# Kernel tuning notes

Hardware: AMD Instinct MI355X
Metric: run time of the kernel (lower is better)

The kernel has to match this reference:

```python
import jax, jax.numpy as jnp
import numpy as np

B, T, C, K = 16, 4096, 64, 1024  # K = codebook rows including pad row 0


def setup_inputs() -> dict:
    key = jax.random.key(0)
    k1, k2, k3 = jax.random.split(key, 3)
    z = jax.random.normal(k1, (B, T, C), dtype=jnp.float32)
    codebook_weight = jax.random.normal(k2, (K, C), dtype=jnp.float32)
    # contiguous valid prefixes of random length (torch loop breaks at first 0)
    lengths = jax.random.randint(k3, (B,), T // 2, T + 1)
    mask = (jnp.arange(T)[None, :] < lengths[:, None]).astype(jnp.float32)[:, :, None]
    return {"z": z, "codebook_weight": codebook_weight, "mask": mask}


def _forward(z, codebook_weight, mask):
    # F.normalize(z, p=2, dim=-1) with eps clamp
    z = z / jnp.clip(jnp.linalg.norm(z, axis=-1, keepdims=True), 1e-12)
    e = jax.lax.stop_gradient(codebook_weight)[1:]  # (K-1, C), detached like torch
    zf = z.reshape(-1, C)                            # (B*T, C)
    # squared euclidean distances: ||z||^2 + ||e||^2 - 2 z e^T
    d = (zf * zf).sum(1, keepdims=True) + (e * e).sum(1)[None, :] - 2.0 * (zf @ e.T)
    idx = jnp.argmin(d, axis=1).reshape(B, T)        # (B, T) codes in [0, K-2]
    # scatter(one-hot) @ e  ==  gather rows of e
    z_q = e[idx] * mask                              # (B, T, C)

    valid_count = mask.sum()
    commitment_loss = (jnp.square(z - jax.lax.stop_gradient(z_q)) * mask).sum() / valid_count

    # straight-through estimator
    z_q = z + z_q - jax.lax.stop_gradient(z)

    m1 = mask[:, 1:, :]
    smoothness_loss = (jnp.square(z_q[:, :-1, :] - z_q[:, 1:, :]) * m1).sum() / m1.sum()

    # --- parallel RLE (replaces the host-side python loop) ---
    # torch loop breaks at first mask==0 -> only contiguous valid prefix matters
    mvalid = jnp.cumprod(mask[..., 0], axis=1) > 0   # (B, T) bool
    change = idx[:, 1:] != idx[:, :-1]
    # position 0 always starts a segment; new segment where code changes inside valid prefix
    is_start = jnp.concatenate(
        [jnp.ones((B, 1), dtype=bool), change & mvalid[:, 1:]], axis=1)  # (B, T)
    # stable argsort puts start positions first, in increasing time order
    order = jnp.argsort(jnp.where(is_start, 0, 1), axis=1)               # (B, T)
    n = is_start.sum(axis=1)                                             # segments per batch
    sel_mask = jnp.arange(T)[None, :] < n[:, None]                        # (B, T)
    sel_pos = jnp.where(sel_mask, order, 0)                               # padded to T
    n_mask = sel_mask.astype(jnp.float32)[..., None]                      # (B, T, 1)
    n_z_q = jnp.take_along_axis(z_q, sel_pos[:, :, None], axis=1) * n_mask
    selected_encodings = jnp.where(
        sel_mask, jnp.take_along_axis(idx, sel_pos, axis=1) + 1, 0)       # (B, T) int
    return smoothness_loss, commitment_loss, z_q, n_z_q, n_mask, selected_encodings


def reference(z, codebook_weight, mask):
    return _forward(z, codebook_weight, mask)
```

## Files before the change

### kernel.cpp

```cpp
#include <hip/hip_runtime.h>
#include <math.h>

typedef __attribute__((ext_vector_type(8))) short short8;
typedef __attribute__((ext_vector_type(4))) float f32x4;

#define B_  16
#define T_  4096
#define C_  64
#define KE_ 1023
#define BT_ (B_ * T_)
#define WINDOW 1e-3f


__device__ __forceinline__ unsigned short f2bf(float x) {
    unsigned int u = __float_as_uint(x);
    unsigned int r = (u + 0x7FFFu + ((u >> 16) & 1u)) >> 16;
    return (unsigned short)r;
}
__device__ __forceinline__ float bf2f(unsigned short h) {
    return __uint_as_float(((unsigned int)h) << 16);
}

__global__ __launch_bounds__(256) void k_prep(const float* __restrict__ cb,
                                              float* __restrict__ ee,
                                              unsigned short* __restrict__ Eh,
                                              unsigned short* __restrict__ El,
                                              int* __restrict__ flagcnt) {
    const int k = blockIdx.x * 256 + threadIdx.x;
    if (k == 0) *flagcnt = 0;
    unsigned int* EhU = (unsigned int*)Eh;
    unsigned int* ElU = (unsigned int*)El;
    if (k < KE_) {
        const float* r = cb + (size_t)(k + 1) * C_;
        float s = 0.f;
        #pragma unroll
        for (int c = 0; c < C_; c += 2) {
            const float x0 = r[c], x1 = r[c + 1];
            s = fmaf(x0, x0, s);
            s = fmaf(x1, x1, s);
            const unsigned short h0 = f2bf(x0), h1 = f2bf(x1);
            const unsigned short l0 = f2bf(x0 - bf2f(h0));
            const unsigned short l1 = f2bf(x1 - bf2f(h1));
            EhU[k * 32 + c / 2] = (unsigned int)h0 | ((unsigned int)h1 << 16);
            ElU[k * 32 + c / 2] = (unsigned int)l0 | ((unsigned int)l1 << 16);
        }
        ee[k] = s;
    } else {
        #pragma unroll
        for (int c = 0; c < 32; ++c) { EhU[k * 32 + c] = 0u; ElU[k * 32 + c] = 0u; }
        ee[k] = INFINITY;
    }
}

__global__ __launch_bounds__(256, 4) void k_assign(
    const float* __restrict__ z, const unsigned short* __restrict__ Eh,
    const unsigned short* __restrict__ El, const float* __restrict__ ee,
    int* __restrict__ kbest, int* __restrict__ flaglist,
    int* __restrict__ flagcnt) {

    __shared__ __align__(16) unsigned short s_eh[128 * 72];
    __shared__ __align__(16) unsigned short s_el[128 * 72];
    __shared__ float s_ee[128];

    const int tid  = threadIdx.x;
    const int wave = tid >> 6;
    const int lane = tid & 63;
    const int col  = lane & 15;
    const int quad = lane >> 4;
    const int Q0   = blockIdx.x * 128 + wave * 32;

    short8 ah[2][2], al[2][2];
    #pragma unroll
    for (int g = 0; g < 2; ++g) {
        const float4* zp = (const float4*)(z + (size_t)(Q0 + g * 16 + col) * C_);
        const float4 f0 = zp[quad * 2];
        const float4 f1 = zp[quad * 2 + 1];
        const float4 f2 = zp[8 + quad * 2];
        const float4 f3 = zp[8 + quad * 2 + 1];
        float xs[16] = {f0.x, f0.y, f0.z, f0.w, f1.x, f1.y, f1.z, f1.w,
                        f2.x, f2.y, f2.z, f2.w, f3.x, f3.y, f3.z, f3.w};
        float ss = 0.f;
        #pragma unroll
        for (int i = 0; i < 16; ++i) ss = fmaf(xs[i], xs[i], ss);
        ss += __shfl_xor(ss, 16);
        ss += __shfl_xor(ss, 32);
        const float inv = 1.f / fmaxf(sqrtf(ss), 1e-12f);
        short8 h0, h1, l0, l1;
        #pragma unroll
        for (int i = 0; i < 8; ++i) {
            const float x = xs[i] * inv;
            const unsigned short hx = f2bf(x);
            h0[i] = (short)hx;
            l0[i] = (short)f2bf(x - bf2f(hx));
            const float y = xs[8 + i] * inv;
            const unsigned short hy = f2bf(y);
            h1[i] = (short)hy;
            l1[i] = (short)f2bf(y - bf2f(hy));
        }
        ah[g][0] = h0; ah[g][1] = h1;
        al[g][0] = l0; al[g][1] = l1;
    }

    float bestv[2][4], secv[2][4];
    int   bkk[2][4];
    #pragma unroll
    for (int g = 0; g < 2; ++g)
        #pragma unroll
        for (int r = 0; r < 4; ++r) {
            bestv[g][r] = INFINITY; secv[g][r] = INFINITY; bkk[g][r] = 0;
        }

    for (int t = 0; t < 8; ++t) {
        __syncthreads();
        #pragma unroll
        for (int j = 0; j < 4; ++j) {
            const int p   = j * 256 + tid;
            const int row = p >> 3;
            const int pc  = p & 7;
            *(uint4*)(&s_eh[row * 72 + pc * 8]) =
                *(const uint4*)(&Eh[(size_t)(t * 128 + row) * 64 + pc * 8]);
            *(uint4*)(&s_el[row * 72 + pc * 8]) =
                *(const uint4*)(&El[(size_t)(t * 128 + row) * 64 + pc * 8]);
        }
        if (tid < 128) s_ee[tid] = ee[t * 128 + tid];
        __syncthreads();

        #pragma unroll 2
        for (int s = 0; s < 8; ++s) {
            const int rbase = (s * 16 + col) * 72 + quad * 8;
            const short8 bh0 = *(const short8*)(&s_eh[rbase]);
            const short8 bh1 = *(const short8*)(&s_eh[rbase + 32]);
            const short8 bl0 = *(const short8*)(&s_el[rbase]);
            const short8 bl1 = *(const short8*)(&s_el[rbase + 32]);
            const float  eev = s_ee[s * 16 + col];

            f32x4 p0 = {0.f, 0.f, 0.f, 0.f}, q0 = {0.f, 0.f, 0.f, 0.f};
            f32x4 p1 = {0.f, 0.f, 0.f, 0.f}, q1 = {0.f, 0.f, 0.f, 0.f};
            p0 = __builtin_amdgcn_mfma_f32_16x16x32_bf16(ah[0][0], bh0, p0, 0, 0, 0);
            p1 = __builtin_amdgcn_mfma_f32_16x16x32_bf16(ah[1][0], bh0, p1, 0, 0, 0);
            q0 = __builtin_amdgcn_mfma_f32_16x16x32_bf16(ah[0][1], bh1, q0, 0, 0, 0);
            q1 = __builtin_amdgcn_mfma_f32_16x16x32_bf16(ah[1][1], bh1, q1, 0, 0, 0);
            p0 = __builtin_amdgcn_mfma_f32_16x16x32_bf16(ah[0][0], bl0, p0, 0, 0, 0);
            p1 = __builtin_amdgcn_mfma_f32_16x16x32_bf16(ah[1][0], bl0, p1, 0, 0, 0);
            q0 = __builtin_amdgcn_mfma_f32_16x16x32_bf16(ah[0][1], bl1, q0, 0, 0, 0);
            q1 = __builtin_amdgcn_mfma_f32_16x16x32_bf16(ah[1][1], bl1, q1, 0, 0, 0);
            p0 = __builtin_amdgcn_mfma_f32_16x16x32_bf16(al[0][0], bh0, p0, 0, 0, 0);
            p1 = __builtin_amdgcn_mfma_f32_16x16x32_bf16(al[1][0], bh0, p1, 0, 0, 0);
            q0 = __builtin_amdgcn_mfma_f32_16x16x32_bf16(al[0][1], bh1, q0, 0, 0, 0);
            q1 = __builtin_amdgcn_mfma_f32_16x16x32_bf16(al[1][1], bh1, q1, 0, 0, 0);

            const int kc = t * 128 + s * 16 + col;
            #pragma unroll
            for (int r = 0; r < 4; ++r) {
                {
                    const float v = fmaf(-2.f, p0[r] + q0[r], eev);
                    const bool lt = v < bestv[0][r];
                    secv[0][r]  = lt ? bestv[0][r] : fminf(secv[0][r], v);
                    bkk[0][r]   = lt ? kc : bkk[0][r];
                    bestv[0][r] = lt ? v : bestv[0][r];
                }
                {
                    const float v = fmaf(-2.f, p1[r] + q1[r], eev);
                    const bool lt = v < bestv[1][r];
                    secv[1][r]  = lt ? bestv[1][r] : fminf(secv[1][r], v);
                    bkk[1][r]   = lt ? kc : bkk[1][r];
                    bestv[1][r] = lt ? v : bestv[1][r];
                }
            }
        }
    }

    #pragma unroll
    for (int g = 0; g < 2; ++g) {
        #pragma unroll
        for (int r = 0; r < 4; ++r) {
            float b  = bestv[g][r], sc = secv[g][r];
            int   k  = bkk[g][r];
            #pragma unroll
            for (int off = 1; off < 16; off <<= 1) {
                const float ob = __shfl_xor(b, off);
                const int   ok = __shfl_xor(k, off);
                const float os = __shfl_xor(sc, off);
                const bool take = (ob < b) || (ob == b && ok < k);
                const float lose = take ? b : ob;
                sc = fminf(fminf(sc, os), lose);
                b  = take ? ob : b;
                k  = take ? ok : k;
            }
            if (col == 0) {
                const int q = Q0 + g * 16 + quad * 4 + r;
                kbest[q] = k;
                if (!(sc - b > WINDOW)) {
                    const int pos = atomicAdd(flagcnt, 1);
                    flaglist[pos] = q;
                }
            }
        }
    }
}

__global__ __launch_bounds__(256) void k_fix(const float* __restrict__ z,
                                             const float* __restrict__ cb,
                                             const float* __restrict__ ee,
                                             const int* __restrict__ flagcnt,
                                             const int* __restrict__ flaglist,
                                             int* __restrict__ kbest) {
    __shared__ float s_z[64];
    __shared__ float s_bv[4];
    __shared__ int   s_bk[4];
    const int tid  = threadIdx.x;
    const int lane = tid & 63;
    const int wave = tid >> 6;
    const int n = *flagcnt;

    for (int i = blockIdx.x; i < n; i += 1024) {
        const int q = flaglist[i];
        __syncthreads();
        if (tid < 16) ((float4*)s_z)[tid] = ((const float4*)(z + (size_t)q * C_))[tid];
        __syncthreads();

        float4 zn[16];
        float ss = 0.f;
        #pragma unroll
        for (int c4 = 0; c4 < 16; ++c4) {
            const float4 v = ((const float4*)s_z)[c4];
            zn[c4] = v;
            ss = fmaf(v.x, v.x, ss); ss = fmaf(v.y, v.y, ss);
            ss = fmaf(v.z, v.z, ss); ss = fmaf(v.w, v.w, ss);
        }
        const float nrm = fmaxf(sqrtf(ss), 1e-12f);
        #pragma unroll
        for (int c4 = 0; c4 < 16; ++c4) {
            zn[c4].x /= nrm; zn[c4].y /= nrm; zn[c4].z /= nrm; zn[c4].w /= nrm;
        }

        const int k0 = tid * 4;
        const float4* e0 = (const float4*)(cb + (size_t)(k0 + 1) * C_);
        const float4* e1 = (const float4*)(cb + (size_t)(k0 + 2) * C_);
        const float4* e2 = (const float4*)(cb + (size_t)(k0 + 3) * C_);
        const float4* e3 = (const float4*)(cb + (size_t)((k0 + 4 <= KE_) ? (k0 + 4) : KE_) * C_);
        float d0 = 0.f, d1 = 0.f, d2 = 0.f, d3 = 0.f;
        #pragma unroll
        for (int c4 = 0; c4 < 16; ++c4) {
            const float4 x = zn[c4];
            const float4 a = e0[c4], b = e1[c4], c = e2[c4], d = e3[c4];
            d0 = fmaf(x.x, a.x, d0); d0 = fmaf(x.y, a.y, d0);
            d0 = fmaf(x.z, a.z, d0); d0 = fmaf(x.w, a.w, d0);
            d1 = fmaf(x.x, b.x, d1); d1 = fmaf(x.y, b.y, d1);
            d1 = fmaf(x.z, b.z, d1); d1 = fmaf(x.w, b.w, d1);
            d2 = fmaf(x.x, c.x, d2); d2 = fmaf(x.y, c.y, d2);
            d2 = fmaf(x.z, c.z, d2); d2 = fmaf(x.w, c.w, d2);
            d3 = fmaf(x.x, d.x, d3); d3 = fmaf(x.y, d.y, d3);
            d3 = fmaf(x.z, d.z, d3); d3 = fmaf(x.w, d.w, d3);
        }
        float bv = INFINITY;
        int   bk = 0;
        float v;
        v = fmaf(-2.f, d0, ee[k0 + 0]); if (v < bv) { bv = v; bk = k0 + 0; }
        v = fmaf(-2.f, d1, ee[k0 + 1]); if (v < bv) { bv = v; bk = k0 + 1; }
        v = fmaf(-2.f, d2, ee[k0 + 2]); if (v < bv) { bv = v; bk = k0 + 2; }
        v = fmaf(-2.f, d3, ee[k0 + 3]); if (v < bv) { bv = v; bk = k0 + 3; }

        #pragma unroll
        for (int off = 32; off > 0; off >>= 1) {
            const float ov = __shfl_down(bv, off);
            const int   ok = __shfl_down(bk, off);
            if (ov < bv || (ov == bv && ok < bk)) { bv = ov; bk = ok; }
        }
        if (lane == 0) { s_bv[wave] = bv; s_bk[wave] = bk; }
        __syncthreads();
        if (tid == 0) {
            float fb = s_bv[0]; int fk = s_bk[0];
            #pragma unroll
            for (int w = 1; w < 4; ++w) {
                if (s_bv[w] < fb || (s_bv[w] == fb && s_bk[w] < fk)) {
                    fb = s_bv[w]; fk = s_bk[w];
                }
            }
            kbest[q] = fk;
        }
    }
}

__global__ __launch_bounds__(256) void k_epi(
    const float* __restrict__ z, const float* __restrict__ cb,
    const float* __restrict__ mask, const int* __restrict__ kbest,
    float* __restrict__ zqo,
    float* __restrict__ commit_part, float* __restrict__ valid_part,
    float* __restrict__ smooth_part) {

    __shared__ float s_red[12];
    const int tid  = threadIdx.x;
    const int lane = tid & 63;
    const int wave = tid >> 6;
    const int q    = blockIdx.x * 256 + tid;

    const int bi = kbest[q];
    const float m     = mask[q];
    const float mnext = (lane != 63) ? mask[q + 1] : 0.f;

    const float4* zp = (const float4*)(z + (size_t)q * C_);
    const float4* er = (const float4*)(cb + (size_t)(bi + 1) * C_);
    float4* zo = (float4*)(zqo + (size_t)q * C_);

    float4 zr[16];
    float ss = 0.f;
    #pragma unroll
    for (int i = 0; i < 16; ++i) {
        float4 v = zp[i];
        zr[i] = v;
        ss = fmaf(v.x, v.x, ss); ss = fmaf(v.y, v.y, ss);
        ss = fmaf(v.z, v.z, ss); ss = fmaf(v.w, v.w, ss);
    }
    const float nrm = fmaxf(sqrtf(ss), 1e-12f);

    float commit = 0.f, sm = 0.f;
    #pragma unroll
    for (int c4 = 0; c4 < 16; ++c4) {
        const float z0 = zr[c4].x / nrm, z1 = zr[c4].y / nrm;
        const float z2 = zr[c4].z / nrm, z3 = zr[c4].w / nrm;
        const float4 e4 = er[c4];
        const float q0 = e4.x * m, q1 = e4.y * m, q2 = e4.z * m, q3 = e4.w * m;
        float4 o;
        o.x = (z0 + q0) - z0;
        o.y = (z1 + q1) - z1;
        o.z = (z2 + q2) - z2;
        o.w = (z3 + q3) - z3;
        zo[c4] = o;
        const float d0 = z0 - q0, d1 = z1 - q1, d2 = z2 - q2, d3 = z3 - q3;
        commit = fmaf(d0, d0, commit); commit = fmaf(d1, d1, commit);
        commit = fmaf(d2, d2, commit); commit = fmaf(d3, d3, commit);
        const float n0 = __shfl_down(o.x, 1);
        const float n1 = __shfl_down(o.y, 1);
        const float n2 = __shfl_down(o.z, 1);
        const float n3 = __shfl_down(o.w, 1);
        const float x0 = o.x - n0, x1 = o.y - n1;
        const float x2 = o.z - n2, x3 = o.w - n3;
        sm = fmaf(x0, x0, sm); sm = fmaf(x1, x1, sm);
        sm = fmaf(x2, x2, sm); sm = fmaf(x3, x3, sm);
    }
    commit *= m;
    sm     *= mnext;
    float vc = m;
    #pragma unroll
    for (int off = 32; off > 0; off >>= 1) {
        commit += __shfl_down(commit, off);
        vc     += __shfl_down(vc, off);
        sm     += __shfl_down(sm, off);
    }
    if (lane == 0) { s_red[wave] = commit; s_red[4 + wave] = vc; s_red[8 + wave] = sm; }
    __syncthreads();
    if (tid == 0) {
        commit_part[blockIdx.x] = s_red[0] + s_red[1] + s_red[2] + s_red[3];
        valid_part[blockIdx.x]  = s_red[4] + s_red[5] + s_red[6] + s_red[7];
        smooth_part[blockIdx.x] = s_red[8] + s_red[9] + s_red[10] + s_red[11];
    }
}

__global__ __launch_bounds__(256) void k_scan(const int* __restrict__ kbest,
                                              const float* __restrict__ mask,
                                              const float* __restrict__ zqo,
                                              int* __restrict__ selpos,
                                              int* __restrict__ nst,
                                              float* __restrict__ smooth_part) {
    __shared__ int cnt[256];
    __shared__ float sred[4];
    const int b = blockIdx.x;
    const int tid = threadIdx.x;
    const int base = b * T_;
    const int t0 = tid * 16;

    int flags = 0, c = 0;
    int prev = (tid == 0) ? -1 : kbest[base + t0 - 1];
    #pragma unroll
    for (int i = 0; i < 16; ++i) {
        const int t = t0 + i;
        const int cur = kbest[base + t];
        const int is = (t == 0) ? 1
                     : ((cur != prev && mask[base + t] > 0.f) ? 1 : 0);
        flags |= is << i;
        c += is;
        prev = cur;
    }
    cnt[tid] = c;
    __syncthreads();
    for (int off = 1; off < 256; off <<= 1) {
        int add = (tid >= off) ? cnt[tid - off] : 0;
        __syncthreads();
        cnt[tid] += add;
        __syncthreads();
    }
    int pos = cnt[tid] - c;
    #pragma unroll
    for (int i = 0; i < 16; ++i) {
        if ((flags >> i) & 1) selpos[base + pos++] = t0 + i;
    }
    if (tid == 255) nst[b] = cnt[255];

    float v = 0.f;
    for (int e = tid; e < 63 * 64; e += 256) {
        const int j = e >> 6, cc = e & 63;
        const int t = j * 64 + 63;
        const int qq = base + t;
        const float d = zqo[(size_t)qq * C_ + cc] - zqo[(size_t)(qq + 1) * C_ + cc];
        v = fmaf(d * mask[qq + 1], d, v);
    }
    #pragma unroll
    for (int off = 32; off > 0; off >>= 1) v += __shfl_down(v, off);
    if ((tid & 63) == 0) sred[tid >> 6] = v;
    __syncthreads();
    if (tid == 0) smooth_part[256 + b] = sred[0] + sred[1] + sred[2] + sred[3];
}

__global__ __launch_bounds__(256) void k_gsel(const float* __restrict__ zqo,
                                              const int* __restrict__ kbest,
                                              const int* __restrict__ selpos,
                                              const int* __restrict__ nst,
                                              const float* __restrict__ commit_part,
                                              const float* __restrict__ valid_part,
                                              const float* __restrict__ smooth_part,
                                              float* __restrict__ nzq,
                                              float* __restrict__ nmask,
                                              float* __restrict__ sel,
                                              float* __restrict__ out) {
    const int gid = blockIdx.x * 256 + threadIdx.x;
    const int b   = gid >> 16;
    const int rem = gid & 65535;
    const int j   = rem >> 4;
    const int c4  = rem & 15;
    const int n   = nst[b];
    float4 v = make_float4(0.f, 0.f, 0.f, 0.f);
    int p = 0;
    if (j < n) {
        p = selpos[b * T_ + j];
        v = ((const float4*)zqo)[((size_t)b * T_ + p) * 16 + c4];
    }
    ((float4*)nzq)[gid] = v;
    if (c4 == 0) {
        float nm = 0.f, s = 0.f;
        if (j < n) { nm = 1.f; s = (float)(kbest[b * T_ + p] + 1); }
        nmask[b * T_ + j] = nm;
        sel[b * T_ + j]   = s;
    }

    if (blockIdx.x == 0) {
        __shared__ double rc[256];
        __shared__ double rv[256];
        __shared__ double rs[256];
        const int tid = threadIdx.x;
        double sc = (double)commit_part[tid];
        double sv = (double)valid_part[tid];
        double ssm = (double)smooth_part[tid];
        if (tid < 16) ssm += (double)smooth_part[256 + tid];
        rc[tid] = sc; rv[tid] = sv; rs[tid] = ssm;
        __syncthreads();
        for (int off = 128; off > 0; off >>= 1) {
            if (tid < off) {
                rc[tid] += rc[tid + off];
                rv[tid] += rv[tid + off];
                rs[tid] += rs[tid + off];
            }
            __syncthreads();
        }
        if (tid == 0) {
            double valid = rv[0];
            out[0] = (float)(rs[0] / (valid - (double)B_));
            out[1] = (float)(rc[0] / valid);
        }
    }
}

extern "C" void kernel_launch(void* const* d_in, const int* in_sizes, int n_in,
                              void* d_out, int out_size, void* d_ws, size_t ws_size,
                              hipStream_t stream) {
    const float* z    = (const float*)d_in[0];
    const float* cb   = (const float*)d_in[1];
    const float* mask = (const float*)d_in[2];
    float* out = (float*)d_out;
    char* ws = (char*)d_ws;

    int*            flagcnt     = (int*)(ws + 0);
    float*          ee          = (float*)(ws + 64);
    unsigned short* Eh          = (unsigned short*)(ws + 4224);
    unsigned short* El          = (unsigned short*)(ws + 135296);
    int*            kbest       = (int*)(ws + 266368);
    int*            selpos      = (int*)(ws + 528512);
    int*            nst         = (int*)(ws + 790656);
    float*          commit_part = (float*)(ws + 791680);
    float*          valid_part  = (float*)(ws + 792704);
    float*          smooth_part = (float*)(ws + 793728);
    int*            flaglist    = (int*)(ws + 794816);

    float* zqo   = out + 2;
    float* nzq   = zqo + (size_t)BT_ * C_;
    float* nmask = nzq + (size_t)BT_ * C_;
    float* sel   = nmask + BT_;

    k_prep  <<<4,    256, 0, stream>>>(cb, ee, Eh, El, flagcnt);
    k_assign<<<512,  256, 0, stream>>>(z, Eh, El, ee, kbest, flaglist, flagcnt);
    k_fix   <<<1024, 256, 0, stream>>>(z, cb, ee, flagcnt, flaglist, kbest);
    k_epi   <<<256,  256, 0, stream>>>(z, cb, mask, kbest, zqo,
                                       commit_part, valid_part, smooth_part);
    k_scan  <<<B_,   256, 0, stream>>>(kbest, mask, zqo, selpos, nst, smooth_part);
    k_gsel  <<<4096, 256, 0, stream>>>(zqo, kbest, selpos, nst,
                                       commit_part, valid_part, smooth_part,
                                       nzq, nmask, sel, out);
}
```

Before: 155.7 us.

## Double-buffer codebook tiles via direct global-to-LDS loads and pack argmin keys

Codebook tiles are now prefetched into a second LDS buffer with global_load_lds while the current tile is consumed. The old padded rows are replaced by an XOR swizzle, and one barrier per tile is removed. The codebook is pre-negated and the MFMA accumulator starts at 0.5+0.5*||e||^2, so distances come out of the MFMA directly. Best and second-best tracking become unsigned min/max on keys that pack the positive float bits with the code index in the low 10 bits. This truncates distance precision, which is absorbed by a wider ambiguity window sent to the fixup kernel. It may flag more rows for the fix pass, and the doubled LDS lowers the occupancy hint to 2.

```diff
diff --git a/kernel.cpp b/kernel.cpp
--- a/kernel.cpp
+++ b/kernel.cpp
@@ -9,7 +9,7 @@
 #define C_  64
 #define KE_ 1023
 #define BT_ (B_ * T_)
-#define WINDOW 1e-3f
+#define WINHALF 0.01f
 
 
 __device__ __forceinline__ unsigned short f2bf(float x) {
@@ -21,8 +21,15 @@
     return __uint_as_float(((unsigned int)h) << 16);
 }
 
+typedef __attribute__((address_space(1))) const unsigned int g_u32;
+typedef __attribute__((address_space(3))) unsigned int l_u32;
+__device__ __forceinline__ void gload16(const void* g, void* l) {
+    __builtin_amdgcn_global_load_lds((g_u32*)g, (l_u32*)l, 16, 0, 0);
+}
+
 __global__ __launch_bounds__(256) void k_prep(const float* __restrict__ cb,
                                               float* __restrict__ ee,
+                                              float* __restrict__ ee2,
                                               unsigned short* __restrict__ Eh,
                                               unsigned short* __restrict__ El,
                                               int* __restrict__ flagcnt) {
@@ -38,29 +45,32 @@
             const float x0 = r[c], x1 = r[c + 1];
             s = fmaf(x0, x0, s);
             s = fmaf(x1, x1, s);
-            const unsigned short h0 = f2bf(x0), h1 = f2bf(x1);
-            const unsigned short l0 = f2bf(x0 - bf2f(h0));
-            const unsigned short l1 = f2bf(x1 - bf2f(h1));
+            const float n0 = -x0, n1 = -x1;
+            const unsigned short h0 = f2bf(n0), h1 = f2bf(n1);
+            const unsigned short l0 = f2bf(n0 - bf2f(h0));
+            const unsigned short l1 = f2bf(n1 - bf2f(h1));
             EhU[k * 32 + c / 2] = (unsigned int)h0 | ((unsigned int)h1 << 16);
             ElU[k * 32 + c / 2] = (unsigned int)l0 | ((unsigned int)l1 << 16);
         }
-        ee[k] = s;
+        ee[k]  = s;
+        ee2[k] = 0.5f + 0.5f * s;
     } else {
         #pragma unroll
         for (int c = 0; c < 32; ++c) { EhU[k * 32 + c] = 0u; ElU[k * 32 + c] = 0u; }
-        ee[k] = INFINITY;
-    }
-}
-
-__global__ __launch_bounds__(256, 4) void k_assign(
+        ee[k]  = INFINITY;
+        ee2[k] = INFINITY;
+    }
+}
+
+__global__ __launch_bounds__(256, 2) void k_assign(
     const float* __restrict__ z, const unsigned short* __restrict__ Eh,
-    const unsigned short* __restrict__ El, const float* __restrict__ ee,
+    const unsigned short* __restrict__ El, const float* __restrict__ ee2,
     int* __restrict__ kbest, int* __restrict__ flaglist,
     int* __restrict__ flagcnt) {
 
-    __shared__ __align__(16) unsigned short s_eh[128 * 72];
-    __shared__ __align__(16) unsigned short s_el[128 * 72];
-    __shared__ float s_ee[128];
+    __shared__ __align__(16) unsigned short s_eh[2][128 * 64];
+    __shared__ __align__(16) unsigned short s_el[2][128 * 64];
+    __shared__ float s_ee[2][128];
 
     const int tid  = threadIdx.x;
     const int wave = tid >> 6;
@@ -101,41 +111,51 @@
         al[g][0] = l0; al[g][1] = l1;
     }
 
-    float bestv[2][4], secv[2][4];
-    int   bkk[2][4];
+    unsigned bK[2][4], sK[2][4];
     #pragma unroll
     for (int g = 0; g < 2; ++g)
         #pragma unroll
-        for (int r = 0; r < 4; ++r) {
-            bestv[g][r] = INFINITY; secv[g][r] = INFINITY; bkk[g][r] = 0;
-        }
+        for (int r = 0; r < 4; ++r) { bK[g][r] = 0xFFFFFFFFu; sK[g][r] = 0xFFFFFFFFu; }
+
+    const int srow = tid >> 3;
+    const int schk = (tid & 7) ^ (srow & 7);
+    const int ldsb = (wave * 8) * 64;
+
+#define STAGE(tt, bb) do {                                                     \
+        _Pragma("unroll")                                                      \
+        for (int j = 0; j < 4; ++j) {                                          \
+            const size_t go = (size_t)((tt) * 128 + j * 32 + srow) * 64        \
+                              + (size_t)schk * 8;                              \
+            gload16(Eh + go, (void*)&s_eh[bb][ldsb + j * 32 * 64]);            \
+            gload16(El + go, (void*)&s_el[bb][ldsb + j * 32 * 64]);            \
+        }                                                                      \
+        if (tid < 128) s_ee[bb][tid] = ee2[(tt) * 128 + tid];                  \
+    } while (0)
+
+    int cur = 0;
+    STAGE(0, 0);
+    __syncthreads();
+
+    const int coff = (quad ^ (col & 7)) * 8;
 
     for (int t = 0; t < 8; ++t) {
-        __syncthreads();
-        #pragma unroll
-        for (int j = 0; j < 4; ++j) {
-            const int p   = j * 256 + tid;
-            const int row = p >> 3;
-            const int pc  = p & 7;
-            *(uint4*)(&s_eh[row * 72 + pc * 8]) =
-                *(const uint4*)(&Eh[(size_t)(t * 128 + row) * 64 + pc * 8]);
-            *(uint4*)(&s_el[row * 72 + pc * 8]) =
-                *(const uint4*)(&El[(size_t)(t * 128 + row) * 64 + pc * 8]);
-        }
-        if (tid < 128) s_ee[tid] = ee[t * 128 + tid];
-        __syncthreads();
+        if (t < 7) STAGE(t + 1, cur ^ 1);
+
+        float ev[8];
+        #pragma unroll
+        for (int s = 0; s < 8; ++s) ev[s] = s_ee[cur][s * 16 + col];
 
         #pragma unroll 2
         for (int s = 0; s < 8; ++s) {
-            const int rbase = (s * 16 + col) * 72 + quad * 8;
-            const short8 bh0 = *(const short8*)(&s_eh[rbase]);
-            const short8 bh1 = *(const short8*)(&s_eh[rbase + 32]);
-            const short8 bl0 = *(const short8*)(&s_el[rbase]);
-            const short8 bl1 = *(const short8*)(&s_el[rbase + 32]);
-            const float  eev = s_ee[s * 16 + col];
-
-            f32x4 p0 = {0.f, 0.f, 0.f, 0.f}, q0 = {0.f, 0.f, 0.f, 0.f};
-            f32x4 p1 = {0.f, 0.f, 0.f, 0.f}, q1 = {0.f, 0.f, 0.f, 0.f};
+            const int rb = (s * 16 + col) * 64;
+            const short8 bh0 = *(const short8*)&s_eh[cur][rb + coff];
+            const short8 bh1 = *(const short8*)&s_eh[cur][rb + (coff ^ 32)];
+            const short8 bl0 = *(const short8*)&s_el[cur][rb + coff];
+            const short8 bl1 = *(const short8*)&s_el[cur][rb + (coff ^ 32)];
+
+            const float e2 = ev[s];
+            f32x4 p0 = {e2, e2, e2, e2}, p1 = {e2, e2, e2, e2};
+            f32x4 q0 = {0.f, 0.f, 0.f, 0.f}, q1 = {0.f, 0.f, 0.f, 0.f};
             p0 = __builtin_amdgcn_mfma_f32_16x16x32_bf16(ah[0][0], bh0, p0, 0, 0, 0);
             p1 = __builtin_amdgcn_mfma_f32_16x16x32_bf16(ah[1][0], bh0, p1, 0, 0, 0);
             q0 = __builtin_amdgcn_mfma_f32_16x16x32_bf16(ah[0][1], bh1, q0, 0, 0, 0);
@@ -149,48 +169,52 @@
             q0 = __builtin_amdgcn_mfma_f32_16x16x32_bf16(al[0][1], bh1, q0, 0, 0, 0);
             q1 = __builtin_amdgcn_mfma_f32_16x16x32_bf16(al[1][1], bh1, q1, 0, 0, 0);
 
-            const int kc = t * 128 + s * 16 + col;
+            const unsigned kc = (unsigned)(t * 128 + s * 16 + col);
             #pragma unroll
             for (int r = 0; r < 4; ++r) {
                 {
-                    const float v = fmaf(-2.f, p0[r] + q0[r], eev);
-                    const bool lt = v < bestv[0][r];
-                    secv[0][r]  = lt ? bestv[0][r] : fminf(secv[0][r], v);
-                    bkk[0][r]   = lt ? kc : bkk[0][r];
-                    bestv[0][r] = lt ? v : bestv[0][r];
+                    const unsigned key =
+                        (__float_as_uint(p0[r] + q0[r]) & 0xFFFFFC00u) | kc;
+                    const unsigned mx = key > bK[0][r] ? key : bK[0][r];
+                    const unsigned mn = key < bK[0][r] ? key : bK[0][r];
+                    sK[0][r] = sK[0][r] < mx ? sK[0][r] : mx;
+                    bK[0][r] = mn;
                 }
                 {
-                    const float v = fmaf(-2.f, p1[r] + q1[r], eev);
-                    const bool lt = v < bestv[1][r];
-                    secv[1][r]  = lt ? bestv[1][r] : fminf(secv[1][r], v);
-                    bkk[1][r]   = lt ? kc : bkk[1][r];
-                    bestv[1][r] = lt ? v : bestv[1][r];
+                    const unsigned key =
+                        (__float_as_uint(p1[r] + q1[r]) & 0xFFFFFC00u) | kc;
+                    const unsigned mx = key > bK[1][r] ? key : bK[1][r];
+                    const unsigned mn = key < bK[1][r] ? key : bK[1][r];
+                    sK[1][r] = sK[1][r] < mx ? sK[1][r] : mx;
+                    bK[1][r] = mn;
                 }
             }
         }
-    }
+        __syncthreads();
+        cur ^= 1;
+    }
+#undef STAGE
 
     #pragma unroll
     for (int g = 0; g < 2; ++g) {
         #pragma unroll
         for (int r = 0; r < 4; ++r) {
-            float b  = bestv[g][r], sc = secv[g][r];
-            int   k  = bkk[g][r];
+            unsigned b = bK[g][r], s2 = sK[g][r];
             #pragma unroll
             for (int off = 1; off < 16; off <<= 1) {
-                const float ob = __shfl_xor(b, off);
-                const int   ok = __shfl_xor(k, off);
-                const float os = __shfl_xor(sc, off);
-                const bool take = (ob < b) || (ob == b && ok < k);
-                const float lose = take ? b : ob;
-                sc = fminf(fminf(sc, os), lose);
-                b  = take ? ob : b;
-                k  = take ? ok : k;
+                const unsigned ob = (unsigned)__shfl_xor((int)b, off);
+                const unsigned os = (unsigned)__shfl_xor((int)s2, off);
+                const unsigned mx = b > ob ? b : ob;
+                const unsigned mns = s2 < os ? s2 : os;
+                s2 = mns < mx ? mns : mx;
+                b  = b < ob ? b : ob;
             }
             if (col == 0) {
                 const int q = Q0 + g * 16 + quad * 4 + r;
-                kbest[q] = k;
-                if (!(sc - b > WINDOW)) {
+                kbest[q] = (int)(b & 1023u);
+                const float bf = __uint_as_float(b  & 0xFFFFFC00u);
+                const float sf = __uint_as_float(s2 & 0xFFFFFC00u);
+                if (!(sf - bf > WINHALF)) {
                     const int pos = atomicAdd(flagcnt, 1);
                     flaglist[pos] = q;
                 }
@@ -490,14 +514,15 @@
     float*          valid_part  = (float*)(ws + 792704);
     float*          smooth_part = (float*)(ws + 793728);
     int*            flaglist    = (int*)(ws + 794816);
+    float*          ee2         = (float*)(ws + 1056960);
 
     float* zqo   = out + 2;
     float* nzq   = zqo + (size_t)BT_ * C_;
     float* nmask = nzq + (size_t)BT_ * C_;
     float* sel   = nmask + BT_;
 
-    k_prep  <<<4,    256, 0, stream>>>(cb, ee, Eh, El, flagcnt);
-    k_assign<<<512,  256, 0, stream>>>(z, Eh, El, ee, kbest, flaglist, flagcnt);
+    k_prep  <<<4,    256, 0, stream>>>(cb, ee, ee2, Eh, El, flagcnt);
+    k_assign<<<512,  256, 0, stream>>>(z, Eh, El, ee2, kbest, flaglist, flagcnt);
     k_fix   <<<1024, 256, 0, stream>>>(z, cb, ee, flagcnt, flaglist, kbest);
     k_epi   <<<256,  256, 0, stream>>>(z, cb, mask, kbest, zqo,
                                        commit_part, valid_part, smooth_part);
```

After: 201.6 us. +29.5%, slower.
